# Kernel tuning notes

Measured on AMD Instinct MI355X. Metric: run time of the kernel, lower is better.

The kernel has to match this reference:

```python
import jax, jax.numpy as jnp
import numpy as np

D_MODEL = 768
NUM_HEADS = 12
D_K = D_MODEL // NUM_HEADS


def setup_inputs() -> dict:
    key = jax.random.key(0)
    ks = jax.random.split(key, 11)
    B, L = 1, 4096
    s = 1.0 / np.sqrt(D_MODEL)
    return {
        "q": jax.random.normal(ks[0], (B, L, D_MODEL), jnp.float32),
        "k": jax.random.normal(ks[1], (B, L, D_MODEL), jnp.float32),
        "v": jax.random.normal(ks[2], (B, L, D_MODEL), jnp.float32),
        "Wq": jax.random.normal(ks[3], (D_MODEL, D_MODEL), jnp.float32) * s,
        "bq": jax.random.normal(ks[4], (D_MODEL,), jnp.float32) * s,
        "Wk": jax.random.normal(ks[5], (D_MODEL, D_MODEL), jnp.float32) * s,
        "bk": jax.random.normal(ks[6], (D_MODEL,), jnp.float32) * s,
        "Wv": jax.random.normal(ks[7], (D_MODEL, D_MODEL), jnp.float32) * s,
        "bv": jax.random.normal(ks[8], (D_MODEL,), jnp.float32) * s,
        "Wo": jax.random.normal(ks[9], (D_MODEL, D_MODEL), jnp.float32) * s,
        "bo": jax.random.normal(ks[10], (D_MODEL,), jnp.float32) * s,
    }


def reference(q, k, v, Wq, bq, Wk, bk, Wv, bv, Wo, bo):
    B, L, _ = q.shape
    # linear projections (torch Linear: x @ W.T + b)
    qp = q @ Wq.T + bq
    kp = k @ Wk.T + bk
    vp = v @ Wv.T + bv
    # split heads: (B, H, L, d_k)
    def split(x):
        return x.reshape(B, L, NUM_HEADS, D_K).transpose(0, 2, 1, 3)
    qh, kh, vh = split(qp), split(kp), split(vp)
    scale = 1.0 / jnp.sqrt(jnp.asarray(D_K, qh.dtype))
    scores = jnp.einsum("bhqd,bhkd->bhqk", qh, kh) * scale  # (B,H,L,L)
    weights = jax.nn.softmax(scores, axis=-1)
    out = jnp.einsum("bhqk,bhkd->bhqd", weights, vh)
    out = out.transpose(0, 2, 1, 3).reshape(B, L, D_MODEL)
    return out @ Wo.T + bo
```

## Files before the change

kernel.cpp:

```cpp
#include <hip/hip_runtime.h>
#include <stdint.h>
#include <math.h>

#define L_SEQ  4096
#define DMODEL 768
#define NHEADS 12
#define DKH    64
#define QSCALE 0.18033688011112042f

typedef _Float16 f16;
typedef __attribute__((ext_vector_type(8))) _Float16 half8;
typedef __attribute__((ext_vector_type(4))) _Float16 half4;
typedef __attribute__((ext_vector_type(4))) float f32x4;
typedef __attribute__((ext_vector_type(16))) float f32x16;
typedef __attribute__((ext_vector_type(4))) unsigned int uint4v;

#define MFMA16(a, b, c) __builtin_amdgcn_mfma_f32_16x16x32_f16(a, b, c, 0, 0, 0)
#define MFMA32(a, b, c) __builtin_amdgcn_mfma_f32_32x32x16_f16(a, b, c, 0, 0, 0)

#define NE ((size_t)L_SEQ * DMODEL)
#define WE ((size_t)DMODEL * DMODEL)

static __device__ __forceinline__ unsigned int pack2(float a, float b) {
  return __builtin_bit_cast(unsigned int, __builtin_amdgcn_cvt_pkrtz(a, b));
}

__global__ __launch_bounds__(256)
void cvt_all(const float* __restrict__ q, const float* __restrict__ k,
             const float* __restrict__ v, const float* __restrict__ Wq,
             const float* __restrict__ Wk, const float* __restrict__ Wv,
             const float* __restrict__ Wo, f16* __restrict__ x16,
             f16* __restrict__ w16)
{
  const size_t NE4 = NE / 4, WE4 = WE / 4;
  size_t i = (size_t)blockIdx.x * 256 + threadIdx.x;
  const float* srcs[7] = {q, k, v, Wq, Wk, Wv, Wo};
  f16* dsts[7] = {x16, x16 + NE, x16 + 2 * NE,
                  w16, w16 + WE, w16 + 2 * WE, w16 + 3 * WE};
  const size_t sz4[7] = {NE4, NE4, NE4, WE4, WE4, WE4, WE4};
  int r = 0; size_t off = i;
  while (off >= sz4[r]) { off -= sz4[r]; ++r; }
  float4 f = reinterpret_cast<const float4*>(srcs[r])[off];
  half4 h; h[0] = (f16)f.x; h[1] = (f16)f.y; h[2] = (f16)f.z; h[3] = (f16)f.w;
  reinterpret_cast<half4*>(dsts[r])[off] = h;
}

__global__ __launch_bounds__(256)
void qkv_gemm(const f16* __restrict__ x16, const f16* __restrict__ w16,
              const float* __restrict__ bq, const float* __restrict__ bk,
              const float* __restrict__ bv,
              f16* __restrict__ Qp, f16* __restrict__ Kp, f16* __restrict__ VpT)
{
  __shared__ f16 As[128][40];
  __shared__ f16 Bs[64][40];
  const int tid  = threadIdx.x;
  const int lane = tid & 63, wid = tid >> 6;
  const int lq   = lane & 15, quad = lane >> 4;
  const int wm   = (wid & 1) * 64, wn = (wid >> 1) * 32;
  const int m0   = blockIdx.y * 128;
  const int widx = blockIdx.x / 12;
  const int n0   = (blockIdx.x % 12) * 64;
  const f16* X = x16 + (size_t)widx * NE;
  const f16* W = w16 + (size_t)widx * WE;
  const float* Bv = (widx == 0) ? bq : (widx == 1) ? bk : bv;

  const int arow = tid >> 1, aseg = (tid & 1) * 16;
  const int brow = tid >> 2, bseg = (tid & 3) * 8;
  const f16* aptr = X + (size_t)(m0 + arow) * DMODEL + aseg;
  const f16* bptr = W + (size_t)(n0 + brow) * DMODEL + bseg;

  half8 a0 = *reinterpret_cast<const half8*>(aptr);
  half8 a1 = *reinterpret_cast<const half8*>(aptr + 8);
  half8 b0 = *reinterpret_cast<const half8*>(bptr);

  f32x4 acc[4][2] = {};

  for (int k0 = 0; k0 < DMODEL; k0 += 32) {
    *reinterpret_cast<half8*>(&As[arow][aseg])     = a0;
    *reinterpret_cast<half8*>(&As[arow][aseg + 8]) = a1;
    *reinterpret_cast<half8*>(&Bs[brow][bseg])     = b0;
    __syncthreads();

    if (k0 + 32 < DMODEL) {
      a0 = *reinterpret_cast<const half8*>(aptr + k0 + 32);
      a1 = *reinterpret_cast<const half8*>(aptr + k0 + 40);
      b0 = *reinterpret_cast<const half8*>(bptr + k0 + 32);
    }

    half8 bf[2];
#pragma unroll
    for (int nf = 0; nf < 2; ++nf)
      bf[nf] = *reinterpret_cast<half8*>(&Bs[wn + nf * 16 + lq][quad * 8]);
#pragma unroll
    for (int mf = 0; mf < 4; ++mf) {
      half8 af = *reinterpret_cast<half8*>(&As[wm + mf * 16 + lq][quad * 8]);
#pragma unroll
      for (int nf = 0; nf < 2; ++nf)
        acc[mf][nf] = MFMA16(af, bf[nf], acc[mf][nf]);
    }
    __syncthreads();
  }

#pragma unroll
  for (int nf = 0; nf < 2; ++nf) {
    const int col  = n0 + wn + nf * 16 + lq;
    const float bias = Bv[col];
#pragma unroll
    for (int mf = 0; mf < 4; ++mf) {
      const int rowb = m0 + wm + mf * 16 + quad * 4;
      if (widx == 2) {
        half4 o4;
#pragma unroll
        for (int r = 0; r < 4; ++r) o4[r] = (f16)(acc[mf][nf][r] + bias);
        *reinterpret_cast<half4*>(VpT + (size_t)col * L_SEQ + rowb) = o4;
      } else if (widx == 0) {
#pragma unroll
        for (int r = 0; r < 4; ++r)
          Qp[(size_t)(rowb + r) * DMODEL + col] = (f16)((acc[mf][nf][r] + bias) * QSCALE);
      } else {
#pragma unroll
        for (int r = 0; r < 4; ++r)
          Kp[(size_t)(rowb + r) * DMODEL + col] = (f16)(acc[mf][nf][r] + bias);
      }
    }
  }
}

__global__ __launch_bounds__(256, 3)
void attn_mfma4(const f16* __restrict__ Qp, const f16* __restrict__ Kp,
                const f16* __restrict__ VpT, f16* __restrict__ AO)
{
  const int h  = blockIdx.x;
  const int q0 = blockIdx.y * 64;
  const int tid  = threadIdx.x;
  const int lane = tid & 63, wid = tid >> 6;
  const int l31  = lane & 31, hc = lane >> 5;
  const int qh   = wid & 1, kh = wid >> 1;

  __shared__ __align__(16) char smem[25088];
  f16 (*Ks)[72] = (f16 (*)[72])smem;
  f16 (*Vt)[72] = (f16 (*)[72])(smem + 9216);
  float* Of  = (float*)smem;
  float* lf  = (float*)(smem + 16384);
  f16*   Of16 = (f16*)(smem + 16640);

  half8 qf[4];
#pragma unroll
  for (int st = 0; st < 4; ++st)
    qf[st] = *reinterpret_cast<const half8*>(
        Qp + (size_t)(q0 + qh * 32 + l31) * DMODEL + h * DKH + st * 16 + hc * 8);

  f32x16 oacc[2] = {};
  float lsum = 0.0f;

  const int srow = tid >> 2, sseg = (tid & 3) * 16;
  const f16* kbase = Kp  + (size_t)srow * DMODEL + h * DKH + sseg;
  const f16* vbase = VpT + (size_t)(h * DKH + srow) * L_SEQ + sseg;

  half8 k0 = *reinterpret_cast<const half8*>(kbase);
  half8 k1 = *reinterpret_cast<const half8*>(kbase + 8);
  half8 v0 = *reinterpret_cast<const half8*>(vbase);
  half8 v1 = *reinterpret_cast<const half8*>(vbase + 8);

  for (int kt = 0; kt < L_SEQ; kt += 64) {
    *reinterpret_cast<half8*>(&Ks[srow][sseg])     = k0;
    *reinterpret_cast<half8*>(&Ks[srow][sseg + 8]) = k1;
    *reinterpret_cast<half8*>(&Vt[srow][sseg])     = v0;
    *reinterpret_cast<half8*>(&Vt[srow][sseg + 8]) = v1;
    __syncthreads();

    if (kt + 64 < L_SEQ) {
      const f16* kn = kbase + (size_t)(kt + 64) * DMODEL;
      const f16* vn = vbase + (kt + 64);
      k0 = *reinterpret_cast<const half8*>(kn);
      k1 = *reinterpret_cast<const half8*>(kn + 8);
      v0 = *reinterpret_cast<const half8*>(vn);
      v1 = *reinterpret_cast<const half8*>(vn + 8);
    }

    f32x16 s = {};
#pragma unroll
    for (int st = 0; st < 4; ++st) {
      half8 kf = *reinterpret_cast<half8*>(&Ks[kh * 32 + l31][st * 16 + hc * 8]);
      s = MFMA32(kf, qf[st], s);
    }

    unsigned int pk[8];
#pragma unroll
    for (int i = 0; i < 8; ++i) {
      float p0 = exp2f(s[2 * i]);
      float p1 = exp2f(s[2 * i + 1]);
      lsum += p0 + p1;
      pk[i] = pack2(p0, p1);
    }

    unsigned int recv[4];
#pragma unroll
    for (int j = 0; j < 4; ++j) {
      unsigned int sv = hc ? pk[(j & 1) + 4 * (j >> 1)]
                           : pk[2 + (j & 1) + 4 * (j >> 1)];
      recv[j] = (unsigned int)__shfl_xor((int)sv, 32);
    }

#pragma unroll
    for (int st = 0; st < 2; ++st) {
      uint4v pw;
#pragma unroll
      for (int t = 0; t < 4; ++t) {
        unsigned int h0v = (t < 2) ? pk[(t & 1) + 4 * st] : recv[2 * st + (t & 1)];
        unsigned int h1v = (t < 2) ? recv[2 * st + (t & 1)] : pk[(t & 1) + 4 * st + 2];
        pw[t] = hc ? h1v : h0v;
      }
      half8 pf = __builtin_bit_cast(half8, pw);
#pragma unroll
      for (int a = 0; a < 2; ++a) {
        half8 vf = *reinterpret_cast<half8*>(&Vt[a * 32 + l31][kh * 32 + st * 16 + hc * 8]);
        oacc[a] = MFMA32(vf, pf, oacc[a]);
      }
    }
    __syncthreads();
  }

  float lw = lsum + __shfl_xor(lsum, 32);

  if (kh == 0) {
#pragma unroll
    for (int a = 0; a < 2; ++a)
#pragma unroll
      for (int r = 0; r < 16; ++r) {
        int d = a * 32 + (r & 3) + 8 * (r >> 2) + 4 * hc;
        Of[((qh * 64) + d) * 32 + l31] = oacc[a][r];
      }
    if (lane < 32) lf[qh * 32 + l31] = lw;
  }
  __syncthreads();
  if (kh == 1) {
    const float inv = 1.0f / (lf[qh * 32 + l31] + lw);
#pragma unroll
    for (int a = 0; a < 2; ++a)
#pragma unroll
      for (int r = 0; r < 16; ++r) {
        int d = a * 32 + (r & 3) + 8 * (r >> 2) + 4 * hc;
        float val = (Of[((qh * 64) + d) * 32 + l31] + oacc[a][r]) * inv;
        Of16[(qh * 32 + l31) * 64 + d] = (f16)val;
      }
  }
  __syncthreads();

  *reinterpret_cast<half8*>(AO + (size_t)(q0 + srow) * DMODEL + h * DKH + sseg) =
      *reinterpret_cast<half8*>(&Of16[srow * 64 + sseg]);
  *reinterpret_cast<half8*>(AO + (size_t)(q0 + srow) * DMODEL + h * DKH + sseg + 8) =
      *reinterpret_cast<half8*>(&Of16[srow * 64 + sseg + 8]);
}

__global__ __launch_bounds__(256)
void out_gemm(const f16* __restrict__ A, const f16* __restrict__ W,
              const float* __restrict__ Bv, float* __restrict__ O)
{
  __shared__ f16 As[64][72];
  __shared__ f16 Bs[64][72];
  const int tid  = threadIdx.x;
  const int lane = tid & 63, wid = tid >> 6;
  const int lq   = lane & 15, quad = lane >> 4;
  const int wm   = (wid & 1) * 32, wn = (wid >> 1) * 32;
  const int m0   = blockIdx.y * 64, n0 = blockIdx.x * 64;

  const int row = tid >> 2, seg = (tid & 3) * 16;
  const f16* aptr = A + (size_t)(m0 + row) * DMODEL + seg;
  const f16* bptr = W + (size_t)(n0 + row) * DMODEL + seg;

  half8 a0 = *reinterpret_cast<const half8*>(aptr);
  half8 a1 = *reinterpret_cast<const half8*>(aptr + 8);
  half8 b0 = *reinterpret_cast<const half8*>(bptr);
  half8 b1 = *reinterpret_cast<const half8*>(bptr + 8);

  f32x4 acc[2][2] = {};

  for (int k0 = 0; k0 < DMODEL; k0 += 64) {
    *reinterpret_cast<half8*>(&As[row][seg])     = a0;
    *reinterpret_cast<half8*>(&As[row][seg + 8]) = a1;
    *reinterpret_cast<half8*>(&Bs[row][seg])     = b0;
    *reinterpret_cast<half8*>(&Bs[row][seg + 8]) = b1;
    __syncthreads();

    if (k0 + 64 < DMODEL) {
      a0 = *reinterpret_cast<const half8*>(aptr + k0 + 64);
      a1 = *reinterpret_cast<const half8*>(aptr + k0 + 72);
      b0 = *reinterpret_cast<const half8*>(bptr + k0 + 64);
      b1 = *reinterpret_cast<const half8*>(bptr + k0 + 72);
    }

#pragma unroll
    for (int ks = 0; ks < 2; ++ks) {
      half8 bf[2];
#pragma unroll
      for (int nf = 0; nf < 2; ++nf)
        bf[nf] = *reinterpret_cast<half8*>(&Bs[wn + nf * 16 + lq][ks * 32 + quad * 8]);
#pragma unroll
      for (int mf = 0; mf < 2; ++mf) {
        half8 af = *reinterpret_cast<half8*>(&As[wm + mf * 16 + lq][ks * 32 + quad * 8]);
#pragma unroll
        for (int nf = 0; nf < 2; ++nf)
          acc[mf][nf] = MFMA16(af, bf[nf], acc[mf][nf]);
      }
    }
    __syncthreads();
  }

#pragma unroll
  for (int nf = 0; nf < 2; ++nf) {
    const int col = n0 + wn + nf * 16 + lq;
    const float bias = Bv[col];
#pragma unroll
    for (int mf = 0; mf < 2; ++mf) {
      const int rowb = m0 + wm + mf * 16 + quad * 4;
#pragma unroll
      for (int r = 0; r < 4; ++r)
        O[(size_t)(rowb + r) * DMODEL + col] = acc[mf][nf][r] + bias;
    }
  }
}

extern "C" void kernel_launch(void* const* d_in, const int* in_sizes, int n_in,
                              void* d_out, int out_size, void* d_ws, size_t ws_size,
                              hipStream_t stream) {
  const float* q  = (const float*)d_in[0];
  const float* k  = (const float*)d_in[1];
  const float* v  = (const float*)d_in[2];
  const float* Wq = (const float*)d_in[3];
  const float* bq = (const float*)d_in[4];
  const float* Wk = (const float*)d_in[5];
  const float* bk = (const float*)d_in[6];
  const float* Wv = (const float*)d_in[7];
  const float* bv = (const float*)d_in[8];
  const float* Wo = (const float*)d_in[9];
  const float* bo = (const float*)d_in[10];
  float* out = (float*)d_out;

  f16* x16 = (f16*)d_ws;
  f16* w16 = x16 + 3 * NE;
  f16* Qp  = w16 + 4 * WE;
  f16* Kp  = Qp + NE;
  f16* VpT = Kp + NE;
  f16* AO  = VpT + NE;

  const int ncvt = (int)((3 * (NE / 4) + 4 * (WE / 4)) / 256);
  cvt_all<<<ncvt, 256, 0, stream>>>(q, k, v, Wq, Wk, Wv, Wo, x16, w16);

  dim3 gqkv(36, L_SEQ / 128);
  qkv_gemm<<<gqkv, 256, 0, stream>>>(x16, w16, bq, bk, bv, Qp, Kp, VpT);

  dim3 gattn(NHEADS, L_SEQ / 64);
  attn_mfma4<<<gattn, 256, 0, stream>>>(Qp, Kp, VpT, AO);

  dim3 gout(DMODEL / 64, L_SEQ / 64);
  out_gemm<<<gout, 256, 0, stream>>>(AO, w16 + 3 * WE, bo, out);
}
```

Measured before the change: 244.3 us.

## Double-buffer attention K/V tiles, use permlane32 swap, and widen QKV GEMM k-step

The attention kernel now keeps two LDS buffers for the K and V tiles, which removes the trailing barrier in each iteration. It raises wave priority around the MFMA work, uses the raw hardware exp2 intrinsic, and replaces the cross-half shuffle of P with v_permlane32_swap. The QKV GEMM moves from a K-step of 32 to 64, halving the number of barriers per tile. In exchange, the attention kernel's LDS use grows to 36 KB, which may reduce occupancy at launch_bounds 3. The unchecked exp2 intrinsic may also differ slightly in accuracy.

```diff
diff --git a/kernel.cpp b/kernel.cpp
--- a/kernel.cpp
+++ b/kernel.cpp
@@ -51,8 +51,8 @@
               const float* __restrict__ bv,
               f16* __restrict__ Qp, f16* __restrict__ Kp, f16* __restrict__ VpT)
 {
-  __shared__ f16 As[128][40];
-  __shared__ f16 Bs[64][40];
+  __shared__ f16 As[128][72];
+  __shared__ f16 Bs[64][72];
   const int tid  = threadIdx.x;
   const int lane = tid & 63, wid = tid >> 6;
   const int lq   = lane & 15, quad = lane >> 4;
@@ -64,39 +64,51 @@
   const f16* W = w16 + (size_t)widx * WE;
   const float* Bv = (widx == 0) ? bq : (widx == 1) ? bk : bv;
 
-  const int arow = tid >> 1, aseg = (tid & 1) * 16;
-  const int brow = tid >> 2, bseg = (tid & 3) * 8;
+  const int arow = tid >> 1, aseg = (tid & 1) * 32;
+  const int brow = tid >> 2, bseg = (tid & 3) * 16;
   const f16* aptr = X + (size_t)(m0 + arow) * DMODEL + aseg;
   const f16* bptr = W + (size_t)(n0 + brow) * DMODEL + bseg;
 
   half8 a0 = *reinterpret_cast<const half8*>(aptr);
   half8 a1 = *reinterpret_cast<const half8*>(aptr + 8);
+  half8 a2 = *reinterpret_cast<const half8*>(aptr + 16);
+  half8 a3 = *reinterpret_cast<const half8*>(aptr + 24);
   half8 b0 = *reinterpret_cast<const half8*>(bptr);
+  half8 b1 = *reinterpret_cast<const half8*>(bptr + 8);
 
   f32x4 acc[4][2] = {};
 
-  for (int k0 = 0; k0 < DMODEL; k0 += 32) {
-    *reinterpret_cast<half8*>(&As[arow][aseg])     = a0;
-    *reinterpret_cast<half8*>(&As[arow][aseg + 8]) = a1;
-    *reinterpret_cast<half8*>(&Bs[brow][bseg])     = b0;
-    __syncthreads();
-
-    if (k0 + 32 < DMODEL) {
-      a0 = *reinterpret_cast<const half8*>(aptr + k0 + 32);
-      a1 = *reinterpret_cast<const half8*>(aptr + k0 + 40);
-      b0 = *reinterpret_cast<const half8*>(bptr + k0 + 32);
-    }
-
-    half8 bf[2];
-#pragma unroll
-    for (int nf = 0; nf < 2; ++nf)
-      bf[nf] = *reinterpret_cast<half8*>(&Bs[wn + nf * 16 + lq][quad * 8]);
-#pragma unroll
-    for (int mf = 0; mf < 4; ++mf) {
-      half8 af = *reinterpret_cast<half8*>(&As[wm + mf * 16 + lq][quad * 8]);
+  for (int k0 = 0; k0 < DMODEL; k0 += 64) {
+    *reinterpret_cast<half8*>(&As[arow][aseg])      = a0;
+    *reinterpret_cast<half8*>(&As[arow][aseg + 8])  = a1;
+    *reinterpret_cast<half8*>(&As[arow][aseg + 16]) = a2;
+    *reinterpret_cast<half8*>(&As[arow][aseg + 24]) = a3;
+    *reinterpret_cast<half8*>(&Bs[brow][bseg])      = b0;
+    *reinterpret_cast<half8*>(&Bs[brow][bseg + 8])  = b1;
+    __syncthreads();
+
+    if (k0 + 64 < DMODEL) {
+      a0 = *reinterpret_cast<const half8*>(aptr + k0 + 64);
+      a1 = *reinterpret_cast<const half8*>(aptr + k0 + 72);
+      a2 = *reinterpret_cast<const half8*>(aptr + k0 + 80);
+      a3 = *reinterpret_cast<const half8*>(aptr + k0 + 88);
+      b0 = *reinterpret_cast<const half8*>(bptr + k0 + 64);
+      b1 = *reinterpret_cast<const half8*>(bptr + k0 + 72);
+    }
+
+#pragma unroll
+    for (int ks = 0; ks < 2; ++ks) {
+      half8 bf[2];
 #pragma unroll
       for (int nf = 0; nf < 2; ++nf)
-        acc[mf][nf] = MFMA16(af, bf[nf], acc[mf][nf]);
+        bf[nf] = *reinterpret_cast<half8*>(&Bs[wn + nf * 16 + lq][ks * 32 + quad * 8]);
+#pragma unroll
+      for (int mf = 0; mf < 4; ++mf) {
+        half8 af = *reinterpret_cast<half8*>(&As[wm + mf * 16 + lq][ks * 32 + quad * 8]);
+#pragma unroll
+        for (int nf = 0; nf < 2; ++nf)
+          acc[mf][nf] = MFMA16(af, bf[nf], acc[mf][nf]);
+      }
     }
     __syncthreads();
   }
@@ -137,9 +149,9 @@
   const int l31  = lane & 31, hc = lane >> 5;
   const int qh   = wid & 1, kh = wid >> 1;
 
-  __shared__ __align__(16) char smem[25088];
-  f16 (*Ks)[72] = (f16 (*)[72])smem;
-  f16 (*Vt)[72] = (f16 (*)[72])(smem + 9216);
+  __shared__ __align__(16) char smem[36864];
+  f16 (*Ks)[64][72] = (f16 (*)[64][72])smem;
+  f16 (*Vt)[64][72] = (f16 (*)[64][72])(smem + 18432);
   float* Of  = (float*)smem;
   float* lf  = (float*)(smem + 16384);
   f16*   Of16 = (f16*)(smem + 16640);
@@ -162,11 +174,12 @@
   half8 v0 = *reinterpret_cast<const half8*>(vbase);
   half8 v1 = *reinterpret_cast<const half8*>(vbase + 8);
 
+  int p = 0;
   for (int kt = 0; kt < L_SEQ; kt += 64) {
-    *reinterpret_cast<half8*>(&Ks[srow][sseg])     = k0;
-    *reinterpret_cast<half8*>(&Ks[srow][sseg + 8]) = k1;
-    *reinterpret_cast<half8*>(&Vt[srow][sseg])     = v0;
-    *reinterpret_cast<half8*>(&Vt[srow][sseg + 8]) = v1;
+    *reinterpret_cast<half8*>(&Ks[p][srow][sseg])     = k0;
+    *reinterpret_cast<half8*>(&Ks[p][srow][sseg + 8]) = k1;
+    *reinterpret_cast<half8*>(&Vt[p][srow][sseg])     = v0;
+    *reinterpret_cast<half8*>(&Vt[p][srow][sseg + 8]) = v1;
     __syncthreads();
 
     if (kt + 64 < L_SEQ) {
@@ -178,48 +191,42 @@
       v1 = *reinterpret_cast<const half8*>(vn + 8);
     }
 
+    __builtin_amdgcn_s_setprio(1);
+
     f32x16 s = {};
 #pragma unroll
     for (int st = 0; st < 4; ++st) {
-      half8 kf = *reinterpret_cast<half8*>(&Ks[kh * 32 + l31][st * 16 + hc * 8]);
+      half8 kf = *reinterpret_cast<half8*>(&Ks[p][kh * 32 + l31][st * 16 + hc * 8]);
       s = MFMA32(kf, qf[st], s);
     }
 
     unsigned int pk[8];
 #pragma unroll
     for (int i = 0; i < 8; ++i) {
-      float p0 = exp2f(s[2 * i]);
-      float p1 = exp2f(s[2 * i + 1]);
+      float p0 = __builtin_amdgcn_exp2f(s[2 * i]);
+      float p1 = __builtin_amdgcn_exp2f(s[2 * i + 1]);
       lsum += p0 + p1;
       pk[i] = pack2(p0, p1);
     }
 
-    unsigned int recv[4];
-#pragma unroll
-    for (int j = 0; j < 4; ++j) {
-      unsigned int sv = hc ? pk[(j & 1) + 4 * (j >> 1)]
-                           : pk[2 + (j & 1) + 4 * (j >> 1)];
-      recv[j] = (unsigned int)__shfl_xor((int)sv, 32);
-    }
-
 #pragma unroll
     for (int st = 0; st < 2; ++st) {
-      uint4v pw;
-#pragma unroll
-      for (int t = 0; t < 4; ++t) {
-        unsigned int h0v = (t < 2) ? pk[(t & 1) + 4 * st] : recv[2 * st + (t & 1)];
-        unsigned int h1v = (t < 2) ? recv[2 * st + (t & 1)] : pk[(t & 1) + 4 * st + 2];
-        pw[t] = hc ? h1v : h0v;
-      }
+      unsigned int w0 = pk[4 * st + 0], w1 = pk[4 * st + 1];
+      unsigned int w2 = pk[4 * st + 2], w3 = pk[4 * st + 3];
+      asm("v_permlane32_swap_b32 %0, %1" : "+v"(w0), "+v"(w2));
+      asm("v_permlane32_swap_b32 %0, %1" : "+v"(w1), "+v"(w3));
+      uint4v pw; pw[0] = w0; pw[1] = w1; pw[2] = w2; pw[3] = w3;
       half8 pf = __builtin_bit_cast(half8, pw);
 #pragma unroll
       for (int a = 0; a < 2; ++a) {
-        half8 vf = *reinterpret_cast<half8*>(&Vt[a * 32 + l31][kh * 32 + st * 16 + hc * 8]);
+        half8 vf = *reinterpret_cast<half8*>(&Vt[p][a * 32 + l31][kh * 32 + st * 16 + hc * 8]);
         oacc[a] = MFMA32(vf, pf, oacc[a]);
       }
     }
-    __syncthreads();
-  }
+    __builtin_amdgcn_s_setprio(0);
+    p ^= 1;
+  }
+  __syncthreads();
 
   float lw = lsum + __shfl_xor(lsum, 32);
 
```

Result: faster. 226.0 us (-7.5%).
